# Performance work log

Hardware: AMD Instinct MI355X
Metric: run time of the kernel (lower is better)

Reference implementation:

```python
import jax, jax.numpy as jnp
import numpy as np

L, D, DFF, H, B, S = 6, 1024, 4096, 16, 4, 512
DK = D // H
EPS = 1e-6


def setup_inputs() -> dict:
    key = jax.random.key(0)
    ks = jax.random.split(key, 20)
    sc = 0.02
    n = jax.random.normal
    return {
        "x": n(ks[0], (B, S, D), jnp.float32),
        "Wq": n(ks[1], (L, D, D)) * sc, "bq": jnp.zeros((L, D)),
        "Wk": n(ks[2], (L, D, D)) * sc, "bk": jnp.zeros((L, D)),
        "Wv": n(ks[3], (L, D, D)) * sc, "bv": jnp.zeros((L, D)),
        "Wo": n(ks[4], (L, D, D)) * sc, "bo": jnp.zeros((L, D)),
        "W1": n(ks[5], (L, D, DFF)) * sc, "b1": jnp.zeros((L, DFF)),
        "W2": n(ks[6], (L, DFF, D)) * sc, "b2": jnp.zeros((L, D)),
        "ln1_a": jnp.ones((L, D)), "ln1_b": jnp.zeros((L, D)),
        "ln2_a": jnp.ones((L, D)), "ln2_b": jnp.zeros((L, D)),
        "norm_a": jnp.ones((D,)), "norm_b": jnp.zeros((D,)),
    }


def _ln(x, a, b):
    # custom LayerNorm: uses sample std (ddof=1, like torch.std) and (std + eps)
    m = x.mean(-1, keepdims=True)
    s = jnp.std(x, axis=-1, ddof=1, keepdims=True)
    return a * (x - m) / (s + EPS) + b


def reference(x, Wq, bq, Wk, bk, Wv, bv, Wo, bo, W1, b1, W2, b2,
              ln1_a, ln1_b, ln2_a, ln2_b, norm_a, norm_b):
    inv = 1.0 / jnp.sqrt(jnp.float32(DK))
    for l in range(L):
        # --- self-attention sublayer (pre-norm, residual) ---
        h = _ln(x, ln1_a[l], ln1_b[l])
        q = (h @ Wq[l] + bq[l]).reshape(B, S, H, DK)
        k = (h @ Wk[l] + bk[l]).reshape(B, S, H, DK)
        v = (h @ Wv[l] + bv[l]).reshape(B, S, H, DK)
        scores = jnp.einsum('bqhd,bkhd->bhqk', q, k) * inv
        p = jax.nn.softmax(scores, axis=-1)
        o = jnp.einsum('bhqk,bkhd->bqhd', p, v).reshape(B, S, D)
        x = x + (o @ Wo[l] + bo[l])
        # --- feed-forward sublayer ---
        h = _ln(x, ln2_a[l], ln2_b[l])
        x = x + (jax.nn.relu(h @ W1[l] + b1[l]) @ W2[l] + b2[l])
    return _ln(x, norm_a, norm_b)
```

## Files before the change

kernel.cpp:

```cpp
#include <hip/hip_runtime.h>
#include <hip/hip_bf16.h>

typedef __hip_bfloat16 bf16;
typedef __bf16 bf16x8 __attribute__((ext_vector_type(8)));
typedef float f32x4 __attribute__((ext_vector_type(4)));

static constexpr int L_ = 6, D_ = 1024, DFF_ = 4096, H_ = 16, B_ = 4, S_ = 512, DK_ = 64;
static constexpr int N_ = B_ * S_;

#define GLOAD_LDS(gp, lp) __builtin_amdgcn_global_load_lds( \
    (const __attribute__((address_space(1))) void*)(gp),    \
    (__attribute__((address_space(3))) void*)(lp), 16, 0, 0)

__global__ void transpose_cast(const float* __restrict__ in, bf16* __restrict__ out,
                               int K, int M, long zin, long zout) {
    const float* ip = in + (size_t)blockIdx.z * zin;
    bf16* op = out + (size_t)blockIdx.z * zout;
    __shared__ float t[32][33];
    int m0 = blockIdx.x * 32, k0 = blockIdx.y * 32;
    int tx = threadIdx.x, ty = threadIdx.y;
    #pragma unroll
    for (int i = 0; i < 32; i += 8)
        t[ty + i][tx] = ip[(size_t)(k0 + ty + i) * M + m0 + tx];
    __syncthreads();
    #pragma unroll
    for (int i = 0; i < 32; i += 8)
        op[(size_t)(m0 + ty + i) * K + k0 + tx] = __float2bfloat16(t[tx][ty + i]);
}

__global__ void pack_qkv_bias(const float* __restrict__ bq, const float* __restrict__ bk,
                              const float* __restrict__ bv, float* __restrict__ out) {
    int t = blockIdx.x * 256 + threadIdx.x;
    int l = t / (3 * D_), c = t % (3 * D_);
    float v = c < D_ ? bq[l * D_ + c] : (c < 2 * D_ ? bk[l * D_ + c - D_] : bv[l * D_ + c - 2 * D_]);
    out[t] = v;
}

template <typename OutT>
__global__ __launch_bounds__(256) void ln_kernel(const float* __restrict__ x,
                                                 const float* __restrict__ ga,
                                                 const float* __restrict__ gb,
                                                 OutT* __restrict__ out) {
    int row = blockIdx.x;
    float4 v = ((const float4*)(x + (size_t)row * D_))[threadIdx.x];
    float s = v.x + v.y + v.z + v.w;
    float q = v.x * v.x + v.y * v.y + v.z * v.z + v.w * v.w;
    #pragma unroll
    for (int m = 1; m < 64; m <<= 1) { s += __shfl_xor(s, m, 64); q += __shfl_xor(q, m, 64); }
    __shared__ float ps[4], pq[4];
    int wid = threadIdx.x >> 6;
    if ((threadIdx.x & 63) == 0) { ps[wid] = s; pq[wid] = q; }
    __syncthreads();
    s = ps[0] + ps[1] + ps[2] + ps[3];
    q = pq[0] + pq[1] + pq[2] + pq[3];
    float mean = s * (1.0f / D_);
    float var = (q - (float)D_ * mean * mean) * (1.0f / (D_ - 1));
    var = var < 0.f ? 0.f : var;
    float rstd = 1.0f / (sqrtf(var) + 1e-6f);
    int c = threadIdx.x * 4;
    float xv[4] = {v.x, v.y, v.z, v.w};
    #pragma unroll
    for (int r = 0; r < 4; r++) {
        float o = ga[c + r] * (xv[r] - mean) * rstd + gb[c + r];
        if constexpr (__hip_internal::is_same<OutT, float>::value)
            out[(size_t)row * D_ + c + r] = o;
        else
            out[(size_t)row * D_ + c + r] = __float2bfloat16(o);
    }
}

template <int S, typename OutT>
__global__ __launch_bounds__(256) void reduce_ln(
    const float* __restrict__ parts, long sK, float* __restrict__ xf,
    const float* __restrict__ ga, const float* __restrict__ gb, OutT* __restrict__ out) {
    int row = blockIdx.x;
    float4 v = ((const float4*)(xf + (size_t)row * D_))[threadIdx.x];
    #pragma unroll
    for (int s = 0; s < S; s++) {
        float4 p = ((const float4*)(parts + (size_t)s * sK + (size_t)row * D_))[threadIdx.x];
        v.x += p.x; v.y += p.y; v.z += p.z; v.w += p.w;
    }
    ((float4*)(xf + (size_t)row * D_))[threadIdx.x] = v;
    float sum = v.x + v.y + v.z + v.w;
    float q = v.x * v.x + v.y * v.y + v.z * v.z + v.w * v.w;
    #pragma unroll
    for (int m = 1; m < 64; m <<= 1) { sum += __shfl_xor(sum, m, 64); q += __shfl_xor(q, m, 64); }
    __shared__ float ps[4], pq[4];
    int wid = threadIdx.x >> 6;
    if ((threadIdx.x & 63) == 0) { ps[wid] = sum; pq[wid] = q; }
    __syncthreads();
    sum = ps[0] + ps[1] + ps[2] + ps[3];
    q = pq[0] + pq[1] + pq[2] + pq[3];
    float mean = sum * (1.0f / D_);
    float var = (q - (float)D_ * mean * mean) * (1.0f / (D_ - 1));
    var = var < 0.f ? 0.f : var;
    float rstd = 1.0f / (sqrtf(var) + 1e-6f);
    int c = threadIdx.x * 4;
    float xv[4] = {v.x, v.y, v.z, v.w};
    #pragma unroll
    for (int r = 0; r < 4; r++) {
        float o = ga[c + r] * (xv[r] - mean) * rstd + gb[c + r];
        if constexpr (__hip_internal::is_same<OutT, float>::value)
            out[(size_t)row * D_ + c + r] = o;
        else
            out[(size_t)row * D_ + c + r] = __float2bfloat16(o);
    }
}

__device__ inline void swz_tiles(int& ntile, int& mtile) {
    unsigned o = blockIdx.y * gridDim.x + blockIdx.x;
    if (gridDim.z == 1) {
        unsigned nwg = gridDim.x * gridDim.y;
        unsigned q = nwg >> 3, r = nwg & 7;
        unsigned xcd = o & 7, j = o >> 3;
        o = (xcd < r ? xcd * (q + 1) : r * (q + 1) + (xcd - r) * q) + j;
    }
    ntile = o % gridDim.x;
    mtile = o / gridDim.x;
}

enum { EPI_RELU = 0, EPI_PART = 1, EPI_QKV = 2 };

template <int EPI, int SPLITK = 1>
__global__ __launch_bounds__(512) void gemm8(
    const bf16* __restrict__ A, int lda,
    const bf16* __restrict__ Bt, int ldb,
    const float* __restrict__ bias,
    void* __restrict__ Cv, int ldc, long sK, int K,
    bf16* __restrict__ qb, bf16* __restrict__ kb, bf16* __restrict__ vT) {
    constexpr int BM = 256, BN = 128, BK = 64;
    constexpr int FM = 4, FN = 4;
    constexpr int IA = BM / 64;
    constexpr int IB = BN / 64;
    __shared__ __align__(16) bf16 As[2][BM * BK];
    __shared__ __align__(16) bf16 Bs[2][BN * BK];
    const int tid = threadIdx.x, wid = tid >> 6, lane = tid & 63;
    const int kz = (SPLITK > 1) ? blockIdx.z : 0;
    int ntile, mtile;
    swz_tiles(ntile, mtile);
    const int m0 = mtile * BM, n0 = ntile * BN;
    const int wm = (wid >> 1) * 64, wn = (wid & 1) * 64;
    const int fr = lane & 15, fg = lane >> 4;
    const int sr = lane >> 3;
    const int c8s = (lane & 7) ^ (sr & 7);
    const int Kc = K / SPLITK;
    const int kbeg = kz * Kc, kend = kbeg + Kc;

    auto stage = [&](int buf, int k0) {
        #pragma unroll
        for (int i = 0; i < IA; i++) {
            int inst = wid * IA + i;
            const bf16* gp = A + (size_t)(m0 + inst * 8 + sr) * lda + k0 + c8s * 8;
            GLOAD_LDS(gp, &As[buf][inst * 512]);
        }
        #pragma unroll
        for (int i = 0; i < IB; i++) {
            int inst = wid * IB + i;
            const bf16* gp = Bt + (size_t)(n0 + inst * 8 + sr) * ldb + k0 + c8s * 8;
            GLOAD_LDS(gp, &Bs[buf][inst * 512]);
        }
    };

    f32x4 acc[FM][FN] = {};
    stage(0, kbeg);
    __syncthreads();
    int cur = 0;
    for (int k0 = kbeg; k0 < kend; k0 += BK) {
        if (k0 + BK < kend) stage(cur ^ 1, k0 + BK);
        #pragma unroll
        for (int kk = 0; kk < 2; kk++) {
            const int cs = ((kk << 2) + fg) ^ (fr & 7);
            bf16x8 af[FM], bfr[FN];
            #pragma unroll
            for (int i = 0; i < FM; i++)
                af[i] = *(const bf16x8*)&As[cur][(wm + i * 16 + fr) * BK + cs * 8];
            #pragma unroll
            for (int j = 0; j < FN; j++)
                bfr[j] = *(const bf16x8*)&Bs[cur][(wn + j * 16 + fr) * BK + cs * 8];
            #pragma unroll
            for (int i = 0; i < FM; i++)
                #pragma unroll
                for (int j = 0; j < FN; j++)
                    acc[i][j] = __builtin_amdgcn_mfma_f32_16x16x32_bf16(af[i], bfr[j], acc[i][j], 0, 0, 0);
        }
        __syncthreads();
        cur ^= 1;
    }
    #pragma unroll
    for (int i = 0; i < FM; i++) {
        #pragma unroll
        for (int j = 0; j < FN; j++) {
            int rr = m0 + wm + i * 16 + (lane >> 4) * 4;
            int cc = n0 + wn + j * 16 + (lane & 15);
            float bv = bias[cc];
            #pragma unroll
            for (int r = 0; r < 4; r++) {
                float v = acc[i][j][r];
                if constexpr (EPI == EPI_RELU) {
                    bf16* C = (bf16*)Cv;
                    float o = v + bv;
                    C[(size_t)(rr + r) * ldc + cc] = __float2bfloat16(o > 0.f ? o : 0.f);
                } else if constexpr (EPI == EPI_PART) {
                    float* C = (float*)Cv;
                    C[(size_t)kz * sK + (size_t)(rr + r) * ldc + cc] = v + (kz == 0 ? bv : 0.f);
                } else {
                    float o = v + bv;
                    if (cc < D_) {
                        qb[(size_t)(rr + r) * D_ + cc] = __float2bfloat16(o);
                    } else if (cc < 2 * D_) {
                        kb[(size_t)(rr + r) * D_ + cc - D_] = __float2bfloat16(o);
                    } else {
                        vT[((size_t)(rr >> 9) * D_ + cc - 2 * D_) * S_ + ((rr & 511) + r)] = __float2bfloat16(o);
                    }
                }
            }
        }
    }
}

__global__ __launch_bounds__(256) void flash_attn(
    const bf16* __restrict__ qb, const bf16* __restrict__ kb, const bf16* __restrict__ vT,
    bf16* __restrict__ ob) {
    __shared__ __align__(16) bf16 P[4][16 * 64];
    const int lane = threadIdx.x & 63, wid = threadIdx.x >> 6;
    const int b = blockIdx.y >> 4, h = blockIdx.y & 15;
    const int q0 = blockIdx.x * 64 + wid * 16;
    const int fr = lane & 15, fg = lane >> 4;
    bf16* Pw = &P[wid][0];

    const bf16* qrow = qb + ((size_t)(b * S_ + q0 + fr)) * D_ + h * DK_ + fg * 8;
    bf16x8 aq0 = *(const bf16x8*)(qrow);
    bf16x8 aq1 = *(const bf16x8*)(qrow + 32);

    f32x4 accO[4] = {};
    float mrow[4] = {-1e30f, -1e30f, -1e30f, -1e30f};
    float lrow[4] = {};

    for (int kv0 = 0; kv0 < S_; kv0 += 64) {
        f32x4 s[4] = {};
        #pragma unroll
        for (int j = 0; j < 4; j++) {
            const bf16* krow = kb + ((size_t)(b * S_ + kv0 + j * 16 + fr)) * D_ + h * DK_ + fg * 8;
            bf16x8 bk0 = *(const bf16x8*)(krow);
            bf16x8 bk1 = *(const bf16x8*)(krow + 32);
            s[j] = __builtin_amdgcn_mfma_f32_16x16x32_bf16(aq0, bk0, s[j], 0, 0, 0);
            s[j] = __builtin_amdgcn_mfma_f32_16x16x32_bf16(aq1, bk1, s[j], 0, 0, 0);
        }
        float tmax[4], alpha[4], rs[4];
        #pragma unroll
        for (int r = 0; r < 4; r++) {
            #pragma unroll
            for (int j = 0; j < 4; j++) s[j][r] *= 0.125f;
            tmax[r] = fmaxf(fmaxf(s[0][r], s[1][r]), fmaxf(s[2][r], s[3][r]));
            #pragma unroll
            for (int m = 1; m < 16; m <<= 1) tmax[r] = fmaxf(tmax[r], __shfl_xor(tmax[r], m, 64));
            float mn = fmaxf(mrow[r], tmax[r]);
            alpha[r] = __expf(mrow[r] - mn);
            mrow[r] = mn;
            rs[r] = 0.f;
        }
        #pragma unroll
        for (int j = 0; j < 4; j++) {
            #pragma unroll
            for (int r = 0; r < 4; r++) {
                float p = __expf(s[j][r] - mrow[r]);
                rs[r] += p;
                int q = fg * 4 + r;
                int col = (j * 16 + fr) ^ ((q & 7) << 3);
                Pw[q * 64 + col] = __float2bfloat16(p);
            }
        }
        #pragma unroll
        for (int r = 0; r < 4; r++) {
            #pragma unroll
            for (int m = 1; m < 16; m <<= 1) rs[r] += __shfl_xor(rs[r], m, 64);
            lrow[r] = lrow[r] * alpha[r] + rs[r];
            #pragma unroll
            for (int j = 0; j < 4; j++) accO[j][r] *= alpha[r];
        }
        #pragma unroll
        for (int ks = 0; ks < 2; ks++) {
            int kk = (ks * 32 + fg * 8) ^ ((fr & 7) << 3);
            bf16x8 ap = *(const bf16x8*)&Pw[fr * 64 + kk];
            #pragma unroll
            for (int j = 0; j < 4; j++) {
                const bf16* vrow = vT + ((size_t)(b * D_) + h * DK_ + j * 16 + fr) * S_ + kv0 + ks * 32 + fg * 8;
                bf16x8 bv = *(const bf16x8*)(vrow);
                accO[j] = __builtin_amdgcn_mfma_f32_16x16x32_bf16(ap, bv, accO[j], 0, 0, 0);
            }
        }
    }
    #pragma unroll
    for (int j = 0; j < 4; j++) {
        #pragma unroll
        for (int r = 0; r < 4; r++) {
            int q = q0 + fg * 4 + r;
            int d = h * DK_ + j * 16 + fr;
            ob[(size_t)(b * S_ + q) * D_ + d] = __float2bfloat16(accO[j][r] / lrow[r]);
        }
    }
}

extern "C" void kernel_launch(void* const* d_in, const int* in_sizes, int n_in,
                              void* d_out, int out_size, void* d_ws, size_t ws_size,
                              hipStream_t stream) {
    (void)in_sizes; (void)n_in; (void)out_size;
    const float* x    = (const float*)d_in[0];
    const float* Wq   = (const float*)d_in[1];
    const float* pbq  = (const float*)d_in[2];
    const float* Wk   = (const float*)d_in[3];
    const float* pbk  = (const float*)d_in[4];
    const float* Wv   = (const float*)d_in[5];
    const float* pbv  = (const float*)d_in[6];
    const float* Wo   = (const float*)d_in[7];
    const float* pbo  = (const float*)d_in[8];
    const float* W1   = (const float*)d_in[9];
    const float* pb1  = (const float*)d_in[10];
    const float* W2   = (const float*)d_in[11];
    const float* pb2  = (const float*)d_in[12];
    const float* l1a  = (const float*)d_in[13];
    const float* l1b  = (const float*)d_in[14];
    const float* l2a  = (const float*)d_in[15];
    const float* l2b  = (const float*)d_in[16];
    const float* nrma = (const float*)d_in[17];
    const float* nrmb = (const float*)d_in[18];

    char* ws = (char*)d_ws;
    size_t off = 0;
    auto alloc = [&](size_t bytes) { void* p = ws + off; off += (bytes + 255) & ~(size_t)255; return p; };
    float* xf  = (float*)alloc((size_t)N_ * D_ * 4);
    bf16* hbuf = (bf16*)alloc((size_t)N_ * D_ * 2);
    bf16* qbuf = (bf16*)alloc((size_t)N_ * D_ * 2);
    bf16* kbuf = (bf16*)alloc((size_t)N_ * D_ * 2);
    bf16* vT   = (bf16*)alloc((size_t)B_ * D_ * S_ * 2);
    bf16* obuf = (bf16*)alloc((size_t)N_ * D_ * 2);
    float* qkvb = (float*)alloc((size_t)L_ * 3 * D_ * 4);
    bf16* mid  = (bf16*)alloc((size_t)N_ * DFF_ * 2);
    float* wsP = (float*)alloc((size_t)4 * N_ * D_ * 4);
    const size_t szDD = (size_t)D_ * D_, szDF = (size_t)D_ * DFF_;
    const long sK = (long)N_ * D_;
    size_t wtFull = (3 * L_ * szDD + L_ * szDD + 2 * L_ * szDF) * 2;
    size_t wtLayer = (4 * szDD + 2 * szDF) * 2;
    bool full = (off + wtFull) <= ws_size;
    bf16* WT = (bf16*)alloc(full ? wtFull : wtLayer);

    pack_qkv_bias<<<L_ * 3 * D_ / 256, 256, 0, stream>>>(pbq, pbk, pbv, qkvb);

    bf16 *Wqkv0, *WoT0, *W1T0, *W2T0;
    dim3 tb(32, 8);
    if (full) {
        Wqkv0 = WT;
        WoT0  = WT + 3 * L_ * szDD;
        W1T0  = WoT0 + L_ * szDD;
        W2T0  = W1T0 + L_ * szDF;
        transpose_cast<<<dim3(D_ / 32, D_ / 32, L_), tb, 0, stream>>>(Wq, Wqkv0, D_, D_, szDD, 3 * szDD);
        transpose_cast<<<dim3(D_ / 32, D_ / 32, L_), tb, 0, stream>>>(Wk, Wqkv0 + szDD, D_, D_, szDD, 3 * szDD);
        transpose_cast<<<dim3(D_ / 32, D_ / 32, L_), tb, 0, stream>>>(Wv, Wqkv0 + 2 * szDD, D_, D_, szDD, 3 * szDD);
        transpose_cast<<<dim3(D_ / 32, D_ / 32, L_), tb, 0, stream>>>(Wo, WoT0, D_, D_, szDD, szDD);
        transpose_cast<<<dim3(DFF_ / 32, D_ / 32, L_), tb, 0, stream>>>(W1, W1T0, D_, DFF_, szDF, szDF);
        transpose_cast<<<dim3(D_ / 32, DFF_ / 32, L_), tb, 0, stream>>>(W2, W2T0, DFF_, D_, szDF, szDF);
    } else {
        Wqkv0 = WT; WoT0 = WT + 3 * szDD; W1T0 = WoT0 + szDD; W2T0 = W1T0 + szDF;
    }

    hipMemcpyAsync(xf, x, (size_t)N_ * D_ * 4, hipMemcpyDeviceToDevice, stream);
    ln_kernel<bf16><<<N_, 256, 0, stream>>>(xf, l1a, l1b, hbuf);

    for (int l = 0; l < L_; l++) {
        const bf16 *WqkvT, *WoT, *W1T, *W2T;
        if (full) {
            WqkvT = Wqkv0 + (size_t)l * 3 * szDD;
            WoT = WoT0 + l * szDD; W1T = W1T0 + l * szDF; W2T = W2T0 + l * szDF;
        } else {
            transpose_cast<<<dim3(D_ / 32, D_ / 32, 1), tb, 0, stream>>>(Wq + l * szDD, Wqkv0, D_, D_, 0, 0);
            transpose_cast<<<dim3(D_ / 32, D_ / 32, 1), tb, 0, stream>>>(Wk + l * szDD, Wqkv0 + szDD, D_, D_, 0, 0);
            transpose_cast<<<dim3(D_ / 32, D_ / 32, 1), tb, 0, stream>>>(Wv + l * szDD, Wqkv0 + 2 * szDD, D_, D_, 0, 0);
            transpose_cast<<<dim3(D_ / 32, D_ / 32, 1), tb, 0, stream>>>(Wo + l * szDD, WoT0, D_, D_, 0, 0);
            transpose_cast<<<dim3(DFF_ / 32, D_ / 32, 1), tb, 0, stream>>>(W1 + l * szDF, W1T0, D_, DFF_, 0, 0);
            transpose_cast<<<dim3(D_ / 32, DFF_ / 32, 1), tb, 0, stream>>>(W2 + l * szDF, W2T0, DFF_, D_, 0, 0);
            WqkvT = Wqkv0; WoT = WoT0; W1T = W1T0; W2T = W2T0;
        }

        gemm8<EPI_QKV><<<dim3(3 * D_ / 128, N_ / 256, 1), 512, 0, stream>>>(
            hbuf, D_, WqkvT, D_, qkvb + (size_t)l * 3 * D_, nullptr, 0, 0, D_, qbuf, kbuf, vT);
        flash_attn<<<dim3(S_ / 64, B_ * H_), 256, 0, stream>>>(qbuf, kbuf, vT, obuf);
        gemm8<EPI_PART, 4><<<dim3(D_ / 128, N_ / 256, 4), 512, 0, stream>>>(
            obuf, D_, WoT, D_, pbo + l * D_, wsP, D_, sK, D_, nullptr, nullptr, nullptr);
        reduce_ln<4, bf16><<<N_, 256, 0, stream>>>(wsP, sK, xf, l2a + l * D_, l2b + l * D_, hbuf);
        gemm8<EPI_RELU><<<dim3(DFF_ / 128, N_ / 256, 1), 512, 0, stream>>>(
            hbuf, D_, W1T, D_, pb1 + l * DFF_, mid, DFF_, 0, D_, nullptr, nullptr, nullptr);
        gemm8<EPI_PART, 4><<<dim3(D_ / 128, N_ / 256, 4), 512, 0, stream>>>(
            mid, DFF_, W2T, DFF_, pb2 + l * D_, wsP, D_, sK, DFF_, nullptr, nullptr, nullptr);
        if (l < L_ - 1)
            reduce_ln<4, bf16><<<N_, 256, 0, stream>>>(wsP, sK, xf, l1a + (l + 1) * D_, l1b + (l + 1) * D_, hbuf);
        else
            reduce_ln<4, float><<<N_, 256, 0, stream>>>(wsP, sK, xf, nrma, nrmb, (float*)d_out);
    }
}
```

Before: 1.161 ms.

## Switch GEMMs to 128x128 single-buffered tiles with column-major XCD swizzle

Replaces the 256x128 double-buffered 512-thread GEMM with a 128x128 single-buffered 256-thread kernel, halving LDS use so more workgroups can be resident per CU. The XCD tile swizzle now gives each XCD a contiguous band of N-tiles and walks M-tiles within it, aiming to improve L2 reuse of the weight tiles. The Wo projection's split-K drops from 4 to 2, with the following reduce adjusted to match. Removing double buffering exposes global-to-LDS load latency behind two barriers per K step, so the kernel now relies on occupancy to hide it.

```diff
diff --git a/kernel.cpp b/kernel.cpp
--- a/kernel.cpp
+++ b/kernel.cpp
@@ -109,31 +109,32 @@
 
 __device__ inline void swz_tiles(int& ntile, int& mtile) {
     unsigned o = blockIdx.y * gridDim.x + blockIdx.x;
-    if (gridDim.z == 1) {
-        unsigned nwg = gridDim.x * gridDim.y;
-        unsigned q = nwg >> 3, r = nwg & 7;
+    if (gridDim.z == 1 && (gridDim.x & 7) == 0) {
         unsigned xcd = o & 7, j = o >> 3;
-        o = (xcd < r ? xcd * (q + 1) : r * (q + 1) + (xcd - r) * q) + j;
-    }
-    ntile = o % gridDim.x;
-    mtile = o / gridDim.x;
+        unsigned cn = gridDim.x >> 3;
+        ntile = xcd * cn + j / gridDim.y;
+        mtile = j % gridDim.y;
+    } else {
+        ntile = o % gridDim.x;
+        mtile = o / gridDim.x;
+    }
 }
 
 enum { EPI_RELU = 0, EPI_PART = 1, EPI_QKV = 2 };
 
 template <int EPI, int SPLITK = 1>
-__global__ __launch_bounds__(512) void gemm8(
+__global__ __launch_bounds__(256) void gemm4(
     const bf16* __restrict__ A, int lda,
     const bf16* __restrict__ Bt, int ldb,
     const float* __restrict__ bias,
     void* __restrict__ Cv, int ldc, long sK, int K,
     bf16* __restrict__ qb, bf16* __restrict__ kb, bf16* __restrict__ vT) {
-    constexpr int BM = 256, BN = 128, BK = 64;
+    constexpr int BM = 128, BN = 128, BK = 64;
     constexpr int FM = 4, FN = 4;
-    constexpr int IA = BM / 64;
-    constexpr int IB = BN / 64;
-    __shared__ __align__(16) bf16 As[2][BM * BK];
-    __shared__ __align__(16) bf16 Bs[2][BN * BK];
+    constexpr int IA = BM / 32;
+    constexpr int IB = BN / 32;
+    __shared__ __align__(16) bf16 As[BM * BK];
+    __shared__ __align__(16) bf16 Bs[BN * BK];
     const int tid = threadIdx.x, wid = tid >> 6, lane = tid & 63;
     const int kz = (SPLITK > 1) ? blockIdx.z : 0;
     int ntile, mtile;
@@ -146,45 +147,38 @@
     const int Kc = K / SPLITK;
     const int kbeg = kz * Kc, kend = kbeg + Kc;
 
-    auto stage = [&](int buf, int k0) {
+    f32x4 acc[FM][FN] = {};
+    for (int k0 = kbeg; k0 < kend; k0 += BK) {
+        __syncthreads();
         #pragma unroll
         for (int i = 0; i < IA; i++) {
             int inst = wid * IA + i;
             const bf16* gp = A + (size_t)(m0 + inst * 8 + sr) * lda + k0 + c8s * 8;
-            GLOAD_LDS(gp, &As[buf][inst * 512]);
+            GLOAD_LDS(gp, &As[inst * 512]);
         }
         #pragma unroll
         for (int i = 0; i < IB; i++) {
             int inst = wid * IB + i;
             const bf16* gp = Bt + (size_t)(n0 + inst * 8 + sr) * ldb + k0 + c8s * 8;
-            GLOAD_LDS(gp, &Bs[buf][inst * 512]);
-        }
-    };
-
-    f32x4 acc[FM][FN] = {};
-    stage(0, kbeg);
-    __syncthreads();
-    int cur = 0;
-    for (int k0 = kbeg; k0 < kend; k0 += BK) {
-        if (k0 + BK < kend) stage(cur ^ 1, k0 + BK);
+            GLOAD_LDS(gp, &Bs[inst * 512]);
+        }
+        __syncthreads();
         #pragma unroll
         for (int kk = 0; kk < 2; kk++) {
             const int cs = ((kk << 2) + fg) ^ (fr & 7);
             bf16x8 af[FM], bfr[FN];
             #pragma unroll
             for (int i = 0; i < FM; i++)
-                af[i] = *(const bf16x8*)&As[cur][(wm + i * 16 + fr) * BK + cs * 8];
+                af[i] = *(const bf16x8*)&As[(wm + i * 16 + fr) * BK + cs * 8];
             #pragma unroll
             for (int j = 0; j < FN; j++)
-                bfr[j] = *(const bf16x8*)&Bs[cur][(wn + j * 16 + fr) * BK + cs * 8];
+                bfr[j] = *(const bf16x8*)&Bs[(wn + j * 16 + fr) * BK + cs * 8];
             #pragma unroll
             for (int i = 0; i < FM; i++)
                 #pragma unroll
                 for (int j = 0; j < FN; j++)
                     acc[i][j] = __builtin_amdgcn_mfma_f32_16x16x32_bf16(af[i], bfr[j], acc[i][j], 0, 0, 0);
         }
-        __syncthreads();
-        cur ^= 1;
     }
     #pragma unroll
     for (int i = 0; i < FM; i++) {
@@ -381,15 +375,15 @@
             WqkvT = Wqkv0; WoT = WoT0; W1T = W1T0; W2T = W2T0;
         }
 
-        gemm8<EPI_QKV><<<dim3(3 * D_ / 128, N_ / 256, 1), 512, 0, stream>>>(
+        gemm4<EPI_QKV><<<dim3(3 * D_ / 128, N_ / 128, 1), 256, 0, stream>>>(
             hbuf, D_, WqkvT, D_, qkvb + (size_t)l * 3 * D_, nullptr, 0, 0, D_, qbuf, kbuf, vT);
         flash_attn<<<dim3(S_ / 64, B_ * H_), 256, 0, stream>>>(qbuf, kbuf, vT, obuf);
-        gemm8<EPI_PART, 4><<<dim3(D_ / 128, N_ / 256, 4), 512, 0, stream>>>(
+        gemm4<EPI_PART, 2><<<dim3(D_ / 128, N_ / 128, 2), 256, 0, stream>>>(
             obuf, D_, WoT, D_, pbo + l * D_, wsP, D_, sK, D_, nullptr, nullptr, nullptr);
-        reduce_ln<4, bf16><<<N_, 256, 0, stream>>>(wsP, sK, xf, l2a + l * D_, l2b + l * D_, hbuf);
-        gemm8<EPI_RELU><<<dim3(DFF_ / 128, N_ / 256, 1), 512, 0, stream>>>(
+        reduce_ln<2, bf16><<<N_, 256, 0, stream>>>(wsP, sK, xf, l2a + l * D_, l2b + l * D_, hbuf);
+        gemm4<EPI_RELU><<<dim3(DFF_ / 128, N_ / 128, 1), 256, 0, stream>>>(
             hbuf, D_, W1T, D_, pb1 + l * DFF_, mid, DFF_, 0, D_, nullptr, nullptr, nullptr);
-        gemm8<EPI_PART, 4><<<dim3(D_ / 128, N_ / 256, 4), 512, 0, stream>>>(
+        gemm4<EPI_PART, 4><<<dim3(D_ / 128, N_ / 128, 4), 256, 0, stream>>>(
             mid, DFF_, W2T, DFF_, pb2 + l * D_, wsP, D_, sK, DFF_, nullptr, nullptr, nullptr);
         if (l < L_ - 1)
             reduce_ln<4, bf16><<<N_, 256, 0, stream>>>(wsP, sK, xf, l1a + (l + 1) * D_, l1b + (l + 1) * D_, hbuf);
```

After: 1.130 ms. -2.7%, faster.
